# Kernel optimization log

Hardware: AMD Instinct MI355X
Metric: run time of the kernel (lower is better)

The kernel has to match this reference:

```python
import jax, jax.numpy as jnp
import numpy as np

E = 64          # num_experts
DIM = 1024      # model dim
HID = 512       # per-expert FFN hidden dim
N = 65536       # total routed tokens (1024 per expert)


def setup_inputs() -> dict:
    key = jax.random.key(0)
    k_x, k1, k2, k3 = jax.random.split(key, 4)
    x = jax.random.normal(k_x, (N, DIM), dtype=jnp.float32)
    # learned params: w1/w3 [E, HID, DIM], w2 [E, DIM, HID] (trunc_normal std 0.02 ~ normal*0.02)
    w1 = jax.random.normal(k1, (E, HID, DIM), dtype=jnp.float32) * 0.02
    w2 = jax.random.normal(k2, (E, DIM, HID), dtype=jnp.float32) * 0.02
    w3 = jax.random.normal(k3, (E, HID, DIM), dtype=jnp.float32) * 0.02
    num_tokens_per_expert = jnp.full((E,), N // E, dtype=jnp.int32)
    return {"x": x, "w1": w1, "w2": w2, "w3": w3,
            "num_tokens_per_expert": num_tokens_per_expert}


def reference(x, w1, w2, w3, num_tokens_per_expert):
    # Grouped-GEMM SwiGLU expert FFN (torch._grouped_mm path, bf16 compute).
    bf16 = jnp.bfloat16
    xb = x.astype(bf16)                                   # [N, DIM]
    g = num_tokens_per_expert                             # [E] int32 group sizes
    w1t = jnp.swapaxes(w1.astype(bf16), 1, 2)             # [E, DIM, HID]
    w3t = jnp.swapaxes(w3.astype(bf16), 1, 2)             # [E, DIM, HID]
    w2t = jnp.swapaxes(w2.astype(bf16), 1, 2)             # [E, HID, DIM]
    h = jax.nn.silu(jax.lax.ragged_dot(xb, w1t, g))       # [N, HID]
    h = h * jax.lax.ragged_dot(xb, w3t, g)                # fused gate
    out = jax.lax.ragged_dot(h, w2t, g)                   # [N, DIM]
    return out.astype(x.dtype)
```

## Files before the change

kernel.cpp:

```cpp
#include <hip/hip_runtime.h>
#include <hip/hip_bf16.h>
#include <stdint.h>

#define NE   64
#define DIM  1024
#define HID  512
#define TPE  1024

typedef __attribute__((ext_vector_type(8)))  __bf16          bf16x8;
typedef __attribute__((ext_vector_type(16))) float           f32x16;
typedef __attribute__((ext_vector_type(8)))  unsigned short  ushort8_t;
typedef __attribute__((ext_vector_type(4)))  float           float4_t;

__device__ __forceinline__ unsigned short f2bf(float f) {
  return __builtin_bit_cast(unsigned short, static_cast<__bf16>(f));
}
__device__ __forceinline__ float bf2f(unsigned short u) {
  unsigned int x = ((unsigned int)u) << 16;
  return __builtin_bit_cast(float, x);
}
__device__ __forceinline__ ushort8_t pack8(float4_t a, float4_t b) {
  ushort8_t r;
  r[0] = f2bf(a[0]); r[1] = f2bf(a[1]); r[2] = f2bf(a[2]); r[3] = f2bf(a[3]);
  r[4] = f2bf(b[0]); r[5] = f2bf(b[1]); r[6] = f2bf(b[2]); r[7] = f2bf(b[3]);
  return r;
}
__device__ __forceinline__ bf16x8 ldsfrag(const unsigned short* p) {
  return __builtin_bit_cast(bf16x8, *reinterpret_cast<const ushort8_t*>(p));
}

__device__ __forceinline__ void barrier_lgkm() {
  asm volatile("s_waitcnt lgkmcnt(0)" ::: "memory");
  __builtin_amdgcn_s_barrier();
}

#define LDK 40

__device__ __forceinline__ int xcd_swizzle(int bid, int nwg) {
  return (bid & 7) * (nwg >> 3) + (bid >> 3);
}

#define P1_NKT (DIM / 32)

__global__ __launch_bounds__(256, 3) void p1_kernel(
    const float* __restrict__ X, const float* __restrict__ W1,
    const float* __restrict__ W3, unsigned short* __restrict__ H) {
  __shared__ __align__(16) unsigned short lA[2][128 * LDK];
  __shared__ __align__(16) unsigned short lB[2][128 * LDK];

  const int tile = xcd_swizzle(blockIdx.x, NE * 8 * 8);
  const int e  = tile >> 6;
  const int tn = (tile >> 3) & 7;
  const int tm = tile & 7;
  const int t  = threadIdx.x;

  const float* gA  = X  + (size_t)(e * TPE + tm * 128) * DIM;
  const float* gW1 = W1 + ((size_t)e * HID + tn * 64) * DIM;
  const float* gW3 = W3 + ((size_t)e * HID + tn * 64) * DIM;

  const int ar = t >> 2, ac = (t & 3) * 8;

  float4_t a0[2][2], a1[2][2];
  float4_t bb[2][2];

  auto load_gA = [&](float4_t (&a)[2][2], int kt) {
#pragma unroll
    for (int i = 0; i < 2; ++i) {
      const size_t o = (size_t)(ar + 64 * i) * DIM + kt * 32 + ac;
      a[i][0] = *reinterpret_cast<const float4_t*>(gA + o);
      a[i][1] = *reinterpret_cast<const float4_t*>(gA + o + 4);
    }
  };
  auto load_gB = [&](int kt) {
    const size_t o = (size_t)ar * DIM + kt * 32 + ac;
    bb[0][0] = *reinterpret_cast<const float4_t*>(gW1 + o);
    bb[0][1] = *reinterpret_cast<const float4_t*>(gW1 + o + 4);
    bb[1][0] = *reinterpret_cast<const float4_t*>(gW3 + o);
    bb[1][1] = *reinterpret_cast<const float4_t*>(gW3 + o + 4);
  };
  auto store_lA = [&](int buf, float4_t (&a)[2][2]) {
#pragma unroll
    for (int i = 0; i < 2; ++i)
      *reinterpret_cast<ushort8_t*>(&lA[buf][(ar + 64 * i) * LDK + ac]) =
          pack8(a[i][0], a[i][1]);
  };
  auto store_lB = [&](int buf) {
    *reinterpret_cast<ushort8_t*>(&lB[buf][ar * LDK + ac]) = pack8(bb[0][0], bb[0][1]);
    *reinterpret_cast<ushort8_t*>(&lB[buf][(ar + 64) * LDK + ac]) = pack8(bb[1][0], bb[1][1]);
  };

  const int lane = t & 63;
  const int wv   = t >> 6;
  const int lr   = lane & 31;
  const int ks   = (lane >> 5) * 8;

  f32x16 acc[4];
#pragma unroll
  for (int n = 0; n < 4; ++n)
#pragma unroll
    for (int i = 0; i < 16; ++i) acc[n][i] = 0.f;

  auto mfma_phase = [&](int buf) {
#pragma unroll
    for (int kk = 0; kk < 2; ++kk) {
      const bf16x8 af = ldsfrag(&lA[buf][(wv * 32 + lr) * LDK + kk * 16 + ks]);
#pragma unroll
      for (int n = 0; n < 4; ++n) {
        const bf16x8 bf = ldsfrag(&lB[buf][(n * 32 + lr) * LDK + kk * 16 + ks]);
        acc[n] = __builtin_amdgcn_mfma_f32_32x32x16_bf16(af, bf, acc[n], 0, 0, 0);
      }
    }
  };

  load_gA(a0, 0);
  load_gB(0);
  load_gA(a1, 1);
  for (int kt = 0; kt < P1_NKT; kt += 2) {
    store_lA(0, a0); store_lB(0);
    if (kt + 2 < P1_NKT) load_gA(a0, kt + 2);
    load_gB(kt + 1);
    barrier_lgkm();
    mfma_phase(0);

    store_lA(1, a1); store_lB(1);
    if (kt + 3 < P1_NKT) load_gA(a1, kt + 3);
    if (kt + 2 < P1_NKT) load_gB(kt + 2);
    barrier_lgkm();
    mfma_phase(1);
  }

  const int tokBase = e * TPE + tm * 128 + wv * 32;
  const int hidBase = tn * 64;
  const int ks4     = (lane >> 5) * 4;
#pragma unroll
  for (int n = 0; n < 2; ++n)
#pragma unroll
    for (int r = 0; r < 16; ++r) {
      const int rr  = (r & 3) + 8 * (r >> 2) + ks4;
      const int tok = tokBase + rr;
      const int hid = hidBase + n * 32 + lr;
      const float av = bf2f(f2bf(acc[n][r]));
      const float bv = bf2f(f2bf(acc[n + 2][r]));
      const float s  = av / (1.0f + __expf(-av));
      H[(size_t)tok * HID + hid] = f2bf(s * bv);
    }
}

#define P2_NKT (HID / 32)

__global__ __launch_bounds__(256, 3) void p2_kernel(
    const unsigned short* __restrict__ Hin, const float* __restrict__ W2,
    float* __restrict__ OUT) {
  __shared__ __align__(16) unsigned short lA[2][128 * LDK];
  __shared__ __align__(16) unsigned short lB[2][128 * LDK];

  const int tile = xcd_swizzle(blockIdx.x, NE * 8 * 8);
  const int e  = tile >> 6;
  const int tn = (tile >> 3) & 7;
  const int tm = tile & 7;
  const int t  = threadIdx.x;

  const unsigned short* gA = Hin + (size_t)(e * TPE + tm * 128) * HID;
  const float*          gB = W2  + ((size_t)e * DIM + tn * 128) * HID;

  const int ar = t >> 2, ac = (t & 3) * 8;

  ushort8_t ha0[2], ha1[2];
  float4_t  wb[2][2];

  auto load_gA = [&](ushort8_t (&ha)[2], int kt) {
#pragma unroll
    for (int i = 0; i < 2; ++i)
      ha[i] = *reinterpret_cast<const ushort8_t*>(
          gA + (size_t)(ar + 64 * i) * HID + kt * 32 + ac);
  };
  auto load_gB = [&](int kt) {
#pragma unroll
    for (int i = 0; i < 2; ++i) {
      const size_t o = (size_t)(ar + 64 * i) * HID + kt * 32 + ac;
      wb[i][0] = *reinterpret_cast<const float4_t*>(gB + o);
      wb[i][1] = *reinterpret_cast<const float4_t*>(gB + o + 4);
    }
  };
  auto store_lA = [&](int buf, ushort8_t (&ha)[2]) {
#pragma unroll
    for (int i = 0; i < 2; ++i)
      *reinterpret_cast<ushort8_t*>(&lA[buf][(ar + 64 * i) * LDK + ac]) = ha[i];
  };
  auto store_lB = [&](int buf) {
#pragma unroll
    for (int i = 0; i < 2; ++i)
      *reinterpret_cast<ushort8_t*>(&lB[buf][(ar + 64 * i) * LDK + ac]) =
          pack8(wb[i][0], wb[i][1]);
  };

  const int lane = t & 63;
  const int wv   = t >> 6;
  const int lr   = lane & 31;
  const int ks   = (lane >> 5) * 8;

  f32x16 acc[4];
#pragma unroll
  for (int n = 0; n < 4; ++n)
#pragma unroll
    for (int i = 0; i < 16; ++i) acc[n][i] = 0.f;

  auto mfma_phase = [&](int buf) {
#pragma unroll
    for (int kk = 0; kk < 2; ++kk) {
      const bf16x8 af = ldsfrag(&lA[buf][(wv * 32 + lr) * LDK + kk * 16 + ks]);
#pragma unroll
      for (int n = 0; n < 4; ++n) {
        const bf16x8 bf = ldsfrag(&lB[buf][(n * 32 + lr) * LDK + kk * 16 + ks]);
        acc[n] = __builtin_amdgcn_mfma_f32_32x32x16_bf16(af, bf, acc[n], 0, 0, 0);
      }
    }
  };

  load_gA(ha0, 0);
  load_gB(0);
  load_gA(ha1, 1);
  for (int kt = 0; kt < P2_NKT; kt += 2) {
    store_lA(0, ha0); store_lB(0);
    if (kt + 2 < P2_NKT) load_gA(ha0, kt + 2);
    load_gB(kt + 1);
    barrier_lgkm();
    mfma_phase(0);

    store_lA(1, ha1); store_lB(1);
    if (kt + 3 < P2_NKT) load_gA(ha1, kt + 3);
    if (kt + 2 < P2_NKT) load_gB(kt + 2);
    barrier_lgkm();
    mfma_phase(1);
  }

  const int tokBase = e * TPE + tm * 128 + wv * 32;
  const int dBase   = tn * 128;
  const int ks4     = (lane >> 5) * 4;
#pragma unroll
  for (int n = 0; n < 4; ++n)
#pragma unroll
    for (int r = 0; r < 16; ++r) {
      const int rr  = (r & 3) + 8 * (r >> 2) + ks4;
      const int tok = tokBase + rr;
      const int d   = dBase + n * 32 + lr;
      OUT[(size_t)tok * DIM + d] = bf2f(f2bf(acc[n][r]));
    }
}

extern "C" void kernel_launch(void* const* d_in, const int* in_sizes, int n_in,
                              void* d_out, int out_size, void* d_ws, size_t ws_size,
                              hipStream_t stream) {
  (void)in_sizes; (void)n_in; (void)out_size; (void)ws_size;
  const float* X  = (const float*)d_in[0];
  const float* W1 = (const float*)d_in[1];
  const float* W2 = (const float*)d_in[2];
  const float* W3 = (const float*)d_in[3];

  unsigned short* H = (unsigned short*)d_ws;
  float* OUT = (float*)d_out;

  p1_kernel<<<dim3(NE * 8 * 8), dim3(256), 0, stream>>>(X, W1, W3, H);
  p2_kernel<<<dim3(NE * 8 * 8), dim3(256), 0, stream>>>(H, W2, OUT);
}
```

Before: 438.0 us.

## Pre-convert inputs to bf16 and use LDS-direct-load 256x256 GEMM kernels

Result: slower. 483.3 us (+10.3%).

```diff
diff --git a/kernel.cpp b/kernel.cpp
--- a/kernel.cpp
+++ b/kernel.cpp
@@ -8,8 +8,10 @@
 #define TPE  1024
 
 typedef __attribute__((ext_vector_type(8)))  __bf16          bf16x8;
+typedef __attribute__((ext_vector_type(4)))  float           f32x4;
 typedef __attribute__((ext_vector_type(16))) float           f32x16;
 typedef __attribute__((ext_vector_type(8)))  unsigned short  ushort8_t;
+typedef __attribute__((ext_vector_type(4)))  unsigned short  ushort4_t;
 typedef __attribute__((ext_vector_type(4)))  float           float4_t;
 
 __device__ __forceinline__ unsigned short f2bf(float f) {
@@ -28,11 +30,15 @@
 __device__ __forceinline__ bf16x8 ldsfrag(const unsigned short* p) {
   return __builtin_bit_cast(bf16x8, *reinterpret_cast<const ushort8_t*>(p));
 }
-
 __device__ __forceinline__ void barrier_lgkm() {
   asm volatile("s_waitcnt lgkmcnt(0)" ::: "memory");
   __builtin_amdgcn_s_barrier();
 }
+typedef __attribute__((address_space(1))) const unsigned int gas_uint;
+typedef __attribute__((address_space(3))) unsigned int las_uint;
+__device__ __forceinline__ void gload16(const void* g, void* l) {
+  __builtin_amdgcn_global_load_lds((gas_uint*)g, (las_uint*)l, 16, 0, 0);
+}
 
 #define LDK 40
 
@@ -40,9 +46,189 @@
   return (bid & 7) * (nwg >> 3) + (bid >> 3);
 }
 
+
+__global__ __launch_bounds__(256) void conv_kernel(
+    const float* __restrict__ X, const float* __restrict__ W1,
+    const float* __restrict__ W3, const float* __restrict__ W2,
+    unsigned short* __restrict__ Xb, unsigned short* __restrict__ WB13,
+    unsigned short* __restrict__ W2b) {
+  const long long total = 20971520LL;
+  const long long stride = (long long)gridDim.x * blockDim.x;
+  for (long long c = blockIdx.x * (long long)blockDim.x + threadIdx.x;
+       c < total; c += stride) {
+    const float* src;
+    unsigned short* dst;
+    if (c < 8388608LL) {
+      src = X + c * 8;
+      dst = Xb + c * 8;
+    } else if (c < 16777216LL) {
+      const long long d = c - 8388608LL;
+      const int eg = (int)(d >> 15);
+      const int rem = (int)(d & 32767);
+      const int r = rem >> 7, c8 = rem & 127;
+      const int e = eg >> 2, g = eg & 3;
+      if (r < 128) src = W1 + ((size_t)e * HID + g * 128 + r) * DIM + c8 * 8;
+      else         src = W3 + ((size_t)e * HID + g * 128 + (r - 128)) * DIM + c8 * 8;
+      dst = WB13 + d * 8;
+    } else {
+      const long long d = c - 16777216LL;
+      src = W2 + d * 8;
+      dst = W2b + d * 8;
+    }
+    float4_t v0 = *reinterpret_cast<const float4_t*>(src);
+    float4_t v1 = *reinterpret_cast<const float4_t*>(src + 4);
+    *reinterpret_cast<ushort8_t*>(dst) = pack8(v0, v1);
+  }
+}
+
+
+#define GEMM_CORE(NT, A_ROWLEN, B_ROWLEN, gA, gB, smem)                        \
+  const int lane = threadIdx.x & 63;                                          \
+  const int wid  = threadIdx.x >> 6;                                          \
+  const int wr   = wid >> 2, wn = wid & 3;                 \
+  const int fr   = lane & 15;                                                 \
+  const int c16b = lane >> 4;                                                 \
+  const int swz  = fr & 7;                                                    \
+  const int s_r  = lane >> 3;                 \
+  const int s_c  = ((lane & 7) ^ s_r) * 8;  \
+  f32x4 acc[8][4];                                                            \
+  _Pragma("unroll") for (int m = 0; m < 8; ++m)                               \
+    _Pragma("unroll") for (int n = 0; n < 4; ++n)                             \
+      _Pragma("unroll") for (int i = 0; i < 4; ++i) acc[m][n][i] = 0.f;       \
+  auto stA = [&](int buf, int kt, int j) {                                    \
+    gload16(gA + (size_t)(j * 8 + s_r) * A_ROWLEN + kt * 64 + s_c,            \
+            &smem[buf][0][j * 512]);                                          \
+  };                                                                          \
+  auto stB = [&](int buf, int kt, int j) {                                    \
+    gload16(gB + (size_t)(j * 8 + s_r) * B_ROWLEN + kt * 64 + s_c,            \
+            &smem[buf][1][j * 512]);                                          \
+  };                                                                          \
+  auto rdA = [&](int buf, int m, int kk) {                                    \
+    const int row = wr * 128 + m * 16 + fr;                                   \
+    return ldsfrag(&smem[buf][0][row * 64 + (((c16b + kk * 4) ^ swz) * 8)]);  \
+  };                                                                          \
+  auto rdB = [&](int buf, int nf, int kk) {                                   \
+    const int row = wn * 64 + nf * 16 + fr;                                   \
+    return ldsfrag(&smem[buf][1][row * 64 + (((c16b + kk * 4) ^ swz) * 8)]);  \
+  };                                                                          \
+  _Pragma("unroll 1") for (int j = 0; j < 4; ++j) { stA(0, 0, wid * 4 + j); } \
+  _Pragma("unroll 1") for (int j = 0; j < 4; ++j) { stB(0, 0, wid * 4 + j); } \
+  for (int kt = 0; kt < NT; ++kt) {                                           \
+    const int buf = kt & 1, sbuf = buf ^ 1;                                   \
+    const bool st = (kt + 1 < NT);                                            \
+    asm volatile("s_waitcnt vmcnt(0)" ::: "memory");                          \
+    __builtin_amdgcn_s_barrier();                                             \
+    asm volatile("" ::: "memory");                                            \
+    bf16x8 af[8];                                                             \
+    _Pragma("unroll") for (int q = 0; q < 4; ++q) {                           \
+      const int kk = q >> 1, nh = q & 1;                                      \
+      if (nh == 0) {                                                          \
+        _Pragma("unroll") for (int m = 0; m < 8; ++m) af[m] = rdA(buf, m, kk);\
+      }                                                                       \
+      bf16x8 bf0 = rdB(buf, nh * 2 + 0, kk);                                  \
+      bf16x8 bf1 = rdB(buf, nh * 2 + 1, kk);                                  \
+      if (st) {                                                               \
+        if (q < 2) { stA(sbuf, kt + 1, wid * 4 + q * 2);                      \
+                     stA(sbuf, kt + 1, wid * 4 + q * 2 + 1); }                \
+        else       { stB(sbuf, kt + 1, wid * 4 + (q - 2) * 2);                \
+                     stB(sbuf, kt + 1, wid * 4 + (q - 2) * 2 + 1); }          \
+      }                                                                       \
+      asm volatile("" ::: "memory");                                          \
+      __builtin_amdgcn_s_barrier();                                           \
+      __builtin_amdgcn_s_setprio(1);                                          \
+      _Pragma("unroll") for (int m = 0; m < 8; ++m) {                         \
+        acc[m][nh * 2 + 0] = __builtin_amdgcn_mfma_f32_16x16x32_bf16(         \
+            af[m], bf0, acc[m][nh * 2 + 0], 0, 0, 0);                         \
+        acc[m][nh * 2 + 1] = __builtin_amdgcn_mfma_f32_16x16x32_bf16(         \
+            af[m], bf1, acc[m][nh * 2 + 1], 0, 0, 0);                         \
+      }                                                                       \
+      __builtin_amdgcn_s_setprio(0);                                          \
+    }                                                                         \
+  }
+
+__global__ __launch_bounds__(512, 2) void p1_fast(
+    const unsigned short* __restrict__ Xb, const unsigned short* __restrict__ WB13,
+    unsigned short* __restrict__ H) {
+  __shared__ __align__(16) unsigned short smem[2][2][256 * 64];
+
+  const int tile = xcd_swizzle(blockIdx.x, NE * 4 * 4);
+  const int e  = tile >> 4;
+  const int g  = (tile >> 2) & 3;
+  const int tm = tile & 3;
+  const unsigned short* gA = Xb   + (size_t)(e * TPE + tm * 256) * DIM;
+  const unsigned short* gB = WB13 + (size_t)(e * 4 + g) * 256 * DIM;
+
+  GEMM_CORE(16, DIM, DIM, gA, gB, smem)
+
+  __builtin_amdgcn_s_barrier();
+  unsigned short* bex = &smem[0][0][0];
+  const int q4 = (lane >> 4) * 4;
+  if (wn >= 2) {
+#pragma unroll
+    for (int m = 0; m < 8; ++m)
+#pragma unroll
+      for (int n = 0; n < 4; ++n) {
+        const int hidl = (wn - 2) * 64 + n * 16 + fr;
+        const int tokl = wr * 128 + m * 16 + q4;
+        ushort4_t v;
+#pragma unroll
+        for (int r = 0; r < 4; ++r) v[r] = f2bf(acc[m][n][r]);
+        *reinterpret_cast<ushort4_t*>(&bex[hidl * 264 + tokl]) = v;
+      }
+  }
+  barrier_lgkm();
+  if (wn < 2) {
+    const int rowbase = e * TPE + tm * 256;
+#pragma unroll
+    for (int m = 0; m < 8; ++m)
+#pragma unroll
+      for (int n = 0; n < 4; ++n) {
+        const int hidl = wn * 64 + n * 16 + fr;
+        const int tokl = wr * 128 + m * 16 + q4;
+        const ushort4_t bv =
+            *reinterpret_cast<const ushort4_t*>(&bex[hidl * 264 + tokl]);
+#pragma unroll
+        for (int r = 0; r < 4; ++r) {
+          const float av = bf2f(f2bf(acc[m][n][r]));
+          const float b  = bf2f(bv[r]);
+          const float s  = av / (1.0f + __expf(-av));
+          H[(size_t)(rowbase + tokl + r) * HID + g * 128 + hidl] = f2bf(s * b);
+        }
+      }
+  }
+}
+
+__global__ __launch_bounds__(512, 2) void p2_fast(
+    const unsigned short* __restrict__ Hb, const unsigned short* __restrict__ W2b,
+    float* __restrict__ OUT) {
+  __shared__ __align__(16) unsigned short smem[2][2][256 * 64];
+
+  const int tile = xcd_swizzle(blockIdx.x, NE * 4 * 4);
+  const int e  = tile >> 4;
+  const int tn = (tile >> 2) & 3;
+  const int tm = tile & 3;
+  const unsigned short* gA = Hb  + (size_t)(e * TPE + tm * 256) * HID;
+  const unsigned short* gB = W2b + (size_t)(e * DIM + tn * 256) * HID;
+
+  GEMM_CORE(8, HID, HID, gA, gB, smem)
+
+  const int q4 = (lane >> 4) * 4;
+  const int rowbase = e * TPE + tm * 256;
+#pragma unroll
+  for (int m = 0; m < 8; ++m)
+#pragma unroll
+    for (int n = 0; n < 4; ++n) {
+      const int d    = tn * 256 + wn * 64 + n * 16 + fr;
+      const int tokl = wr * 128 + m * 16 + q4;
+#pragma unroll
+      for (int r = 0; r < 4; ++r)
+        OUT[(size_t)(rowbase + tokl + r) * DIM + d] = bf2f(f2bf(acc[m][n][r]));
+    }
+}
+
 #define P1_NKT (DIM / 32)
 
-__global__ __launch_bounds__(256, 3) void p1_kernel(
+__global__ __launch_bounds__(256, 3) void p1_fb(
     const float* __restrict__ X, const float* __restrict__ W1,
     const float* __restrict__ W3, unsigned short* __restrict__ H) {
   __shared__ __align__(16) unsigned short lA[2][128 * LDK];
@@ -57,12 +243,9 @@
   const float* gA  = X  + (size_t)(e * TPE + tm * 128) * DIM;
   const float* gW1 = W1 + ((size_t)e * HID + tn * 64) * DIM;
   const float* gW3 = W3 + ((size_t)e * HID + tn * 64) * DIM;
-
   const int ar = t >> 2, ac = (t & 3) * 8;
 
-  float4_t a0[2][2], a1[2][2];
-  float4_t bb[2][2];
-
+  float4_t a0[2][2], a1[2][2], bb[2][2];
   auto load_gA = [&](float4_t (&a)[2][2], int kt) {
 #pragma unroll
     for (int i = 0; i < 2; ++i) {
@@ -89,11 +272,7 @@
     *reinterpret_cast<ushort8_t*>(&lB[buf][(ar + 64) * LDK + ac]) = pack8(bb[1][0], bb[1][1]);
   };
 
-  const int lane = t & 63;
-  const int wv   = t >> 6;
-  const int lr   = lane & 31;
-  const int ks   = (lane >> 5) * 8;
-
+  const int lane = t & 63, wv = t >> 6, lr = lane & 31, ks = (lane >> 5) * 8;
   f32x16 acc[4];
 #pragma unroll
   for (int n = 0; n < 4; ++n)
@@ -112,43 +291,39 @@
     }
   };
 
-  load_gA(a0, 0);
-  load_gB(0);
-  load_gA(a1, 1);
+  load_gA(a0, 0); load_gB(0); load_gA(a1, 1);
   for (int kt = 0; kt < P1_NKT; kt += 2) {
     store_lA(0, a0); store_lB(0);
     if (kt + 2 < P1_NKT) load_gA(a0, kt + 2);
     load_gB(kt + 1);
     barrier_lgkm();
     mfma_phase(0);
-
     store_lA(1, a1); store_lB(1);
     if (kt + 3 < P1_NKT) load_gA(a1, kt + 3);
     if (kt + 2 < P1_NKT) load_gB(kt + 2);
     barrier_lgkm();
     mfma_phase(1);
   }
-
   const int tokBase = e * TPE + tm * 128 + wv * 32;
   const int hidBase = tn * 64;
-  const int ks4     = (lane >> 5) * 4;
+  const int ks4 = (lane >> 5) * 4;
 #pragma unroll
   for (int n = 0; n < 2; ++n)
 #pragma unroll
     for (int r = 0; r < 16; ++r) {
-      const int rr  = (r & 3) + 8 * (r >> 2) + ks4;
+      const int rr = (r & 3) + 8 * (r >> 2) + ks4;
       const int tok = tokBase + rr;
       const int hid = hidBase + n * 32 + lr;
       const float av = bf2f(f2bf(acc[n][r]));
       const float bv = bf2f(f2bf(acc[n + 2][r]));
-      const float s  = av / (1.0f + __expf(-av));
+      const float s = av / (1.0f + __expf(-av));
       H[(size_t)tok * HID + hid] = f2bf(s * bv);
     }
 }
 
 #define P2_NKT (HID / 32)
 
-__global__ __launch_bounds__(256, 3) void p2_kernel(
+__global__ __launch_bounds__(256, 3) void p2_fb(
     const unsigned short* __restrict__ Hin, const float* __restrict__ W2,
     float* __restrict__ OUT) {
   __shared__ __align__(16) unsigned short lA[2][128 * LDK];
@@ -162,12 +337,10 @@
 
   const unsigned short* gA = Hin + (size_t)(e * TPE + tm * 128) * HID;
   const float*          gB = W2  + ((size_t)e * DIM + tn * 128) * HID;
-
   const int ar = t >> 2, ac = (t & 3) * 8;
 
   ushort8_t ha0[2], ha1[2];
   float4_t  wb[2][2];
-
   auto load_gA = [&](ushort8_t (&ha)[2], int kt) {
 #pragma unroll
     for (int i = 0; i < 2; ++i)
@@ -194,11 +367,7 @@
           pack8(wb[i][0], wb[i][1]);
   };
 
-  const int lane = t & 63;
-  const int wv   = t >> 6;
-  const int lr   = lane & 31;
-  const int ks   = (lane >> 5) * 8;
-
+  const int lane = t & 63, wv = t >> 6, lr = lane & 31, ks = (lane >> 5) * 8;
   f32x16 acc[4];
 #pragma unroll
   for (int n = 0; n < 4; ++n)
@@ -217,49 +386,55 @@
     }
   };
 
-  load_gA(ha0, 0);
-  load_gB(0);
-  load_gA(ha1, 1);
+  load_gA(ha0, 0); load_gB(0); load_gA(ha1, 1);
   for (int kt = 0; kt < P2_NKT; kt += 2) {
     store_lA(0, ha0); store_lB(0);
     if (kt + 2 < P2_NKT) load_gA(ha0, kt + 2);
     load_gB(kt + 1);
     barrier_lgkm();
     mfma_phase(0);
-
     store_lA(1, ha1); store_lB(1);
     if (kt + 3 < P2_NKT) load_gA(ha1, kt + 3);
     if (kt + 2 < P2_NKT) load_gB(kt + 2);
     barrier_lgkm();
     mfma_phase(1);
   }
-
   const int tokBase = e * TPE + tm * 128 + wv * 32;
-  const int dBase   = tn * 128;
-  const int ks4     = (lane >> 5) * 4;
+  const int dBase = tn * 128;
+  const int ks4 = (lane >> 5) * 4;
 #pragma unroll
   for (int n = 0; n < 4; ++n)
 #pragma unroll
     for (int r = 0; r < 16; ++r) {
-      const int rr  = (r & 3) + 8 * (r >> 2) + ks4;
-      const int tok = tokBase + rr;
-      const int d   = dBase + n * 32 + lr;
-      OUT[(size_t)tok * DIM + d] = bf2f(f2bf(acc[n][r]));
+      const int rr = (r & 3) + 8 * (r >> 2) + ks4;
+      OUT[(size_t)(tokBase + rr) * DIM + dBase + n * 32 + lr] =
+          bf2f(f2bf(acc[n][r]));
     }
 }
 
 extern "C" void kernel_launch(void* const* d_in, const int* in_sizes, int n_in,
                               void* d_out, int out_size, void* d_ws, size_t ws_size,
                               hipStream_t stream) {
-  (void)in_sizes; (void)n_in; (void)out_size; (void)ws_size;
+  (void)in_sizes; (void)n_in; (void)out_size;
   const float* X  = (const float*)d_in[0];
   const float* W1 = (const float*)d_in[1];
   const float* W2 = (const float*)d_in[2];
   const float* W3 = (const float*)d_in[3];
-
-  unsigned short* H = (unsigned short*)d_ws;
   float* OUT = (float*)d_out;
 
-  p1_kernel<<<dim3(NE * 8 * 8), dim3(256), 0, stream>>>(X, W1, W3, H);
-  p2_kernel<<<dim3(NE * 8 * 8), dim3(256), 0, stream>>>(H, W2, OUT);
-}
+  const size_t MiB = 1024 * 1024;
+  if (ws_size >= 384 * MiB) {
+    unsigned short* Xb   = (unsigned short*)d_ws;
+    unsigned short* WB13 = Xb + (size_t)128 * MiB / 2;
+    unsigned short* W2b  = Xb + (size_t)256 * MiB / 2;
+    unsigned short* H    = Xb + (size_t)320 * MiB / 2;
+    conv_kernel<<<dim3(2048), dim3(256), 0, stream>>>(X, W1, W3, W2,
+                                                      Xb, WB13, W2b);
+    p1_fast<<<dim3(NE * 4 * 4), dim3(512), 0, stream>>>(Xb, WB13, H);
+    p2_fast<<<dim3(NE * 4 * 4), dim3(512), 0, stream>>>(H, W2b, OUT);
+  } else {
+    unsigned short* H = (unsigned short*)d_ws;
+    p1_fb<<<dim3(NE * 8 * 8), dim3(256), 0, stream>>>(X, W1, W3, H);
+    p2_fb<<<dim3(NE * 8 * 8), dim3(256), 0, stream>>>(H, W2, OUT);
+  }
+}
```
